# Kernel tuning notes

Measured on AMD Instinct MI355X. Metric: run time of the kernel, lower is better.

## Reference

```python
import jax, jax.numpy as jnp
import numpy as np

C, S, H = 64, 2048, 512
ITERATIONS = 3

def squash(x, eps=1e-07):
    # per-vector squash along last dim: (|x|^2/(1+|x|^2)) * x/|x|
    sq = jnp.sum(x * x, axis=-1, keepdims=True)
    safe_norm = jnp.sqrt(sq + eps)
    scale = sq / (1.0 + sq)
    return scale * (x / safe_norm)

def setup_inputs() -> dict:
    key = jax.random.key(0)
    k1, k2 = jax.random.split(key)
    x = jax.random.normal(k1, (C * S, H), dtype=jnp.float32)
    # xavier-normal init for Linear(H, H)
    std = np.sqrt(2.0 / (H + H)).astype(np.float32)
    W_weight = jax.random.normal(k2, (H, H), dtype=jnp.float32) * std
    W_bias = jnp.zeros((H,), dtype=jnp.float32)
    return {"x": x, "W_weight": W_weight, "W_bias": W_bias}

def reference(x, W_weight, W_bias):
    xr = x.reshape(C, S, H)
    # e_ij = squash(Linear(x))  -> [C, S, H]
    e_ij = squash(jnp.einsum('csh,oh->cso', xr, W_weight) + W_bias)
    b_ij = jnp.zeros((C, S), dtype=x.dtype)
    c_i = jnp.zeros((C, H), dtype=x.dtype)
    for _ in range(ITERATIONS):
        d_i = jax.nn.softmax(b_ij, axis=1)[..., None]          # [C, S, 1]
        c_i = squash(jnp.sum(d_i * e_ij, axis=1))              # [C, H]
        b_ij = b_ij + jnp.einsum('csh,ch->cs', e_ij, c_i)      # [C, S]
    return c_i
```

## Files before the change

kernel.cpp:

```cpp
#include <hip/hip_runtime.h>
#include <hip/hip_fp16.h>

#define HDIM 512

typedef __fp16 fp16x2 __attribute__((ext_vector_type(2)));
typedef _Float16 h8 __attribute__((ext_vector_type(8)));
typedef __attribute__((ext_vector_type(4))) float floatx4;

__global__ __launch_bounds__(256) void prep_w_kernel(
    const float* __restrict__ W, _Float16* __restrict__ wf) {
  int i = (blockIdx.x * 256 + threadIdx.x) * 4;
  float4 f = *(const float4*)(W + i);
  wf[i + 0] = (_Float16)f.x;
  wf[i + 1] = (_Float16)f.y;
  wf[i + 2] = (_Float16)f.z;
  wf[i + 3] = (_Float16)f.w;
}

#define BM 128
#define BN 128
#define BK 64

__global__ __launch_bounds__(256) void gemm_kernel(
    const float* __restrict__ x, const _Float16* __restrict__ wf,
    const float* __restrict__ bias, __half* __restrict__ y,
    float* __restrict__ sq) {
  __shared__ _Float16 xs[BM * BK];
  __shared__ _Float16 wsm[BN * BK];

  const int tid = threadIdx.x;
  const int lane = tid & 63;
  const int widx = tid >> 6;
  const int wave_m = widx >> 1, wave_n = widx & 1;
  const int lrow = lane & 15, quad = lane >> 4, l7 = lane & 7;

  const int bid = blockIdx.x;
  const int m_blk = ((bid >> 5) << 3) + (bid & 7);
  const int n_blk = (bid >> 3) & 3;
  const int row0 = m_blk * BM;
  const int col0 = n_blk * BN;

  floatx4 acc[4][4];
#pragma unroll
  for (int i = 0; i < 4; ++i)
#pragma unroll
    for (int j = 0; j < 4; ++j) acc[i][j] = (floatx4){0.f, 0.f, 0.f, 0.f};

  const int xm = tid >> 3;
  const int xkg = tid & 7;
  const int wn_sub = lane >> 3;
  const int wphys = lane & 7;

  for (int kt = 0; kt < 8; ++kt) {
    const int k0 = kt * BK;
    __syncthreads();
#pragma unroll
    for (int p = 0; p < 4; ++p) {
      int m = p * 32 + xm;
      const float* gp = x + (size_t)(row0 + m) * HDIM + k0 + xkg * 8;
      float4 f0 = *(const float4*)gp;
      float4 f1 = *(const float4*)(gp + 4);
      union { h8 v8; fp16x2 v2[4]; } u;
      u.v2[0] = __builtin_amdgcn_cvt_pkrtz(f0.x, f0.y);
      u.v2[1] = __builtin_amdgcn_cvt_pkrtz(f0.z, f0.w);
      u.v2[2] = __builtin_amdgcn_cvt_pkrtz(f1.x, f1.y);
      u.v2[3] = __builtin_amdgcn_cvt_pkrtz(f1.z, f1.w);
      int phys = xkg ^ (m & 7);
      *(h8*)&xs[m * 64 + phys * 8] = u.v8;
    }
#pragma unroll
    for (int q = 0; q < 4; ++q) {
      int i = widx * 4 + q;
      int n_loc = 8 * i + wn_sub;
      int kg_l = wphys ^ (n_loc & 7);
      size_t goff = (size_t)(col0 + n_loc) * HDIM + k0 + kg_l * 8;
      __builtin_amdgcn_global_load_lds(
          (const __attribute__((address_space(1))) void*)(wf + goff),
          (__attribute__((address_space(3))) void*)&wsm[i * 512], 16, 0, 0);
    }
    __syncthreads();
#pragma unroll
    for (int ks = 0; ks < 2; ++ks) {
      int physA = (ks * 4 + quad) ^ l7;
      h8 a[4], bh[4];
#pragma unroll
      for (int mt = 0; mt < 4; ++mt) {
        int r = wave_m * 64 + mt * 16 + lrow;
        a[mt] = *(const h8*)&xs[r * 64 + physA * 8];
      }
#pragma unroll
      for (int nt = 0; nt < 4; ++nt) {
        int c = wave_n * 64 + nt * 16 + lrow;
        bh[nt] = *(const h8*)&wsm[c * 64 + physA * 8];
      }
#pragma unroll
      for (int mt = 0; mt < 4; ++mt)
#pragma unroll
        for (int nt = 0; nt < 4; ++nt)
          acc[mt][nt] = __builtin_amdgcn_mfma_f32_16x16x32_f16(
              a[mt], bh[nt], acc[mt][nt], 0, 0, 0);
    }
  }

  int colg[4];
  float bias_v[4];
#pragma unroll
  for (int nt = 0; nt < 4; ++nt) {
    colg[nt] = col0 + wave_n * 64 + nt * 16 + lrow;
    bias_v[nt] = bias[colg[nt]];
  }
#pragma unroll
  for (int mt = 0; mt < 4; ++mt) {
#pragma unroll
    for (int r = 0; r < 4; ++r) {
      int rowg = row0 + wave_m * 64 + mt * 16 + quad * 4 + r;
      float s = 0.f;
#pragma unroll
      for (int nt = 0; nt < 4; ++nt) {
        float yv = acc[mt][nt][r] + bias_v[nt];
        s += yv * yv;
        y[(size_t)rowg * HDIM + colg[nt]] = __float2half(yv);
      }
      s += __shfl_xor(s, 1, 64);
      s += __shfl_xor(s, 2, 64);
      s += __shfl_xor(s, 4, 64);
      s += __shfl_xor(s, 8, 64);
      if (lrow == 0) atomicAdd(&sq[rowg], s);
    }
  }
}

__global__ __launch_bounds__(256) void kbv_kernel(
    const __half* __restrict__ y, const float* __restrict__ sqbuf,
    float* __restrict__ b, const float* __restrict__ c_buf,
    float* __restrict__ u_part, float* __restrict__ den_part) {
  const int wave_g = blockIdx.x * 4 + (threadIdx.x >> 6);
  const int lane = threadIdx.x & 63;
  const int cap = wave_g >> 6;
  const int chunk = wave_g & 63;
  const int r0 = cap * 2048 + chunk * 32;

  float c8[8];
  {
    const float4* cp = (const float4*)(c_buf + cap * HDIM + lane * 8);
    float4 ca = cp[0], cb = cp[1];
    c8[0] = ca.x; c8[1] = ca.y; c8[2] = ca.z; c8[3] = ca.w;
    c8[4] = cb.x; c8[5] = cb.y; c8[6] = cb.z; c8[7] = cb.w;
  }
  float u8[8] = {0, 0, 0, 0, 0, 0, 0, 0};
  float den = 0.f;

  union U { int4 v; __half hh[8]; };
  U cur[4], nxt[4];
  const __half* yb = y + (size_t)r0 * HDIM + lane * 8;
#pragma unroll
  for (int j = 0; j < 4; ++j) cur[j].v = *(const int4*)(yb + (size_t)j * HDIM);

  for (int g = 0; g < 8; ++g) {
    const int rg = r0 + g * 4;
    if (g < 7) {
#pragma unroll
      for (int j = 0; j < 4; ++j)
        nxt[j].v = *(const int4*)(yb + (size_t)(g * 4 + 4 + j) * HDIM);
    }
    float sc[4], bv[4];
#pragma unroll
    for (int j = 0; j < 4; ++j) {
      float s = sqbuf[rg + j];
      sc[j] = s / ((1.f + s) * sqrtf(s + 1e-7f));
      bv[j] = b[rg + j];
    }
    float dot[4];
#pragma unroll
    for (int j = 0; j < 4; ++j) {
      float d = 0.f;
#pragma unroll
      for (int k = 0; k < 8; ++k) d += __half2float(cur[j].hh[k]) * c8[k];
      dot[j] = d;
    }
#pragma unroll
    for (int s = 1; s < 64; s <<= 1) {
#pragma unroll
      for (int j = 0; j < 4; ++j) dot[j] += __shfl_xor(dot[j], s, 64);
    }
#pragma unroll
    for (int j = 0; j < 4; ++j) {
      float bn = bv[j] + sc[j] * dot[j];
      if (lane == 0) b[rg + j] = bn;
      float w = __expf(bn);
      den += w;
      float wsc = w * sc[j];
#pragma unroll
      for (int k = 0; k < 8; ++k) u8[k] += wsc * __half2float(cur[j].hh[k]);
    }
#pragma unroll
    for (int j = 0; j < 4; ++j) cur[j] = nxt[j];
  }
  float* up = u_part + (size_t)(cap * 64 + chunk) * HDIM + lane * 8;
  *(float4*)up = (float4){u8[0], u8[1], u8[2], u8[3]};
  *(float4*)(up + 4) = (float4){u8[4], u8[5], u8[6], u8[7]};
  if (lane == 0) den_part[cap * 64 + chunk] = den;
}

__global__ __launch_bounds__(512) void kcsq_kernel(
    const float* __restrict__ u_part, const float* __restrict__ den_part,
    float* __restrict__ out) {
  const int cap = blockIdx.x;
  const int t = threadIdx.x;
  __shared__ float red[512];

  float d = (t < 64) ? den_part[cap * 64 + t] : 0.f;
  red[t] = d;
  __syncthreads();
  for (int s = 256; s > 0; s >>= 1) {
    if (t < s) red[t] += red[t + s];
    __syncthreads();
  }
  const float den = red[0];
  __syncthreads();

  float v = 0.f;
  const float* up = u_part + (size_t)cap * 64 * HDIM + t;
  for (int ch = 0; ch < 64; ++ch) v += up[ch * HDIM];
  v /= den;

  red[t] = v * v;
  __syncthreads();
  for (int s = 256; s > 0; s >>= 1) {
    if (t < s) red[t] += red[t + s];
    __syncthreads();
  }
  const float sqv = red[0];
  const float scv = sqv / ((1.f + sqv) * sqrtf(sqv + 1e-7f));
  out[cap * HDIM + t] = v * scv;
}

extern "C" void kernel_launch(void* const* d_in, const int* in_sizes, int n_in,
                              void* d_out, int out_size, void* d_ws,
                              size_t ws_size, hipStream_t stream) {
  const float* x = (const float*)d_in[0];
  const float* W = (const float*)d_in[1];
  const float* bias = (const float*)d_in[2];
  float* out = (float*)d_out;
  char* ws = (char*)d_ws;

  __half* y = (__half*)ws;
  float* sq = (float*)(ws + (size_t)134217728);
  float* b = sq + 131072;
  float* c_buf = b + 131072;
  _Float16* wf = (_Float16*)(c_buf + 32768);
  float* u_part = (float*)(wf + 262144);
  float* den_part = u_part + (size_t)64 * 64 * 512;

  (void)hipMemsetAsync(sq, 0,
                       (size_t)(131072 + 131072 + 32768) * sizeof(float),
                       stream);

  prep_w_kernel<<<256, 256, 0, stream>>>(W, wf);
  gemm_kernel<<<4096, 256, 0, stream>>>(x, wf, bias, y, sq);

  for (int it = 0; it < 3; ++it) {
    kbv_kernel<<<1024, 256, 0, stream>>>(y, sq, b, c_buf, u_part, den_part);
    kcsq_kernel<<<64, 512, 0, stream>>>(u_part, den_part,
                                        (it == 2) ? out : c_buf);
  }
}
```

Before: 549.6 us.

## Prefetch next GEMM K-tile, widen kbv row batches, reduce partials in-block

The GEMM now double-buffers the weight tile in LDS and holds the next x tile in registers, so global loads for step k+1 overlap the MFMA work of step k. The routing kernel processes 8 rows per group, fully unrolled, which raises memory-level parallelism. It also sums its four waves' partial u vectors in shared memory before writing, which cuts the partial buffer and the final reduction by a factor of 4. The cost is more registers (prefetched x plus 8-row buffers) and more LDS, which may lower occupancy.

```diff
diff --git a/kernel.cpp b/kernel.cpp
--- a/kernel.cpp
+++ b/kernel.cpp
@@ -17,16 +17,12 @@
   wf[i + 3] = (_Float16)f.w;
 }
 
-#define BM 128
-#define BN 128
-#define BK 64
-
 __global__ __launch_bounds__(256) void gemm_kernel(
     const float* __restrict__ x, const _Float16* __restrict__ wf,
     const float* __restrict__ bias, __half* __restrict__ y,
     float* __restrict__ sq) {
-  __shared__ _Float16 xs[BM * BK];
-  __shared__ _Float16 wsm[BN * BK];
+  __shared__ _Float16 xs[128 * 64];
+  __shared__ _Float16 wsm[2][128 * 64];
 
   const int tid = threadIdx.x;
   const int lane = tid & 63;
@@ -37,8 +33,8 @@
   const int bid = blockIdx.x;
   const int m_blk = ((bid >> 5) << 3) + (bid & 7);
   const int n_blk = (bid >> 3) & 3;
-  const int row0 = m_blk * BM;
-  const int col0 = n_blk * BN;
+  const int row0 = m_blk * 128;
+  const int col0 = n_blk * 128;
 
   floatx4 acc[4][4];
 #pragma unroll
@@ -51,34 +47,60 @@
   const int wn_sub = lane >> 3;
   const int wphys = lane & 7;
 
+  float4 xr[4][2];
+  const float* xbase = x + (size_t)row0 * HDIM + xkg * 8;
+#pragma unroll
+  for (int p = 0; p < 4; ++p) {
+    const float* gp = xbase + (size_t)(p * 32 + xm) * HDIM;
+    xr[p][0] = *(const float4*)gp;
+    xr[p][1] = *(const float4*)(gp + 4);
+  }
+#pragma unroll
+  for (int q = 0; q < 4; ++q) {
+    int i = widx * 4 + q;
+    int n_loc = 8 * i + wn_sub;
+    int kg_l = wphys ^ (n_loc & 7);
+    size_t goff = (size_t)(col0 + n_loc) * HDIM + kg_l * 8;
+    __builtin_amdgcn_global_load_lds(
+        (const __attribute__((address_space(1))) void*)(wf + goff),
+        (__attribute__((address_space(3))) void*)&wsm[0][i * 512], 16, 0, 0);
+  }
+
   for (int kt = 0; kt < 8; ++kt) {
-    const int k0 = kt * BK;
     __syncthreads();
 #pragma unroll
     for (int p = 0; p < 4; ++p) {
       int m = p * 32 + xm;
-      const float* gp = x + (size_t)(row0 + m) * HDIM + k0 + xkg * 8;
-      float4 f0 = *(const float4*)gp;
-      float4 f1 = *(const float4*)(gp + 4);
       union { h8 v8; fp16x2 v2[4]; } u;
-      u.v2[0] = __builtin_amdgcn_cvt_pkrtz(f0.x, f0.y);
-      u.v2[1] = __builtin_amdgcn_cvt_pkrtz(f0.z, f0.w);
-      u.v2[2] = __builtin_amdgcn_cvt_pkrtz(f1.x, f1.y);
-      u.v2[3] = __builtin_amdgcn_cvt_pkrtz(f1.z, f1.w);
+      u.v2[0] = __builtin_amdgcn_cvt_pkrtz(xr[p][0].x, xr[p][0].y);
+      u.v2[1] = __builtin_amdgcn_cvt_pkrtz(xr[p][0].z, xr[p][0].w);
+      u.v2[2] = __builtin_amdgcn_cvt_pkrtz(xr[p][1].x, xr[p][1].y);
+      u.v2[3] = __builtin_amdgcn_cvt_pkrtz(xr[p][1].z, xr[p][1].w);
       int phys = xkg ^ (m & 7);
       *(h8*)&xs[m * 64 + phys * 8] = u.v8;
     }
-#pragma unroll
-    for (int q = 0; q < 4; ++q) {
-      int i = widx * 4 + q;
-      int n_loc = 8 * i + wn_sub;
-      int kg_l = wphys ^ (n_loc & 7);
-      size_t goff = (size_t)(col0 + n_loc) * HDIM + k0 + kg_l * 8;
-      __builtin_amdgcn_global_load_lds(
-          (const __attribute__((address_space(1))) void*)(wf + goff),
-          (__attribute__((address_space(3))) void*)&wsm[i * 512], 16, 0, 0);
-    }
     __syncthreads();
+    if (kt < 7) {
+      const int k1 = (kt + 1) * 64;
+      _Float16* wdst = &wsm[(kt + 1) & 1][0];
+#pragma unroll
+      for (int q = 0; q < 4; ++q) {
+        int i = widx * 4 + q;
+        int n_loc = 8 * i + wn_sub;
+        int kg_l = wphys ^ (n_loc & 7);
+        size_t goff = (size_t)(col0 + n_loc) * HDIM + k1 + kg_l * 8;
+        __builtin_amdgcn_global_load_lds(
+            (const __attribute__((address_space(1))) void*)(wf + goff),
+            (__attribute__((address_space(3))) void*)&wdst[i * 512], 16, 0, 0);
+      }
+#pragma unroll
+      for (int p = 0; p < 4; ++p) {
+        const float* gp = xbase + (size_t)(p * 32 + xm) * HDIM + k1;
+        xr[p][0] = *(const float4*)gp;
+        xr[p][1] = *(const float4*)(gp + 4);
+      }
+    }
+    const _Float16* wcur = &wsm[kt & 1][0];
 #pragma unroll
     for (int ks = 0; ks < 2; ++ks) {
       int physA = (ks * 4 + quad) ^ l7;
@@ -91,7 +113,7 @@
 #pragma unroll
       for (int nt = 0; nt < 4; ++nt) {
         int c = wave_n * 64 + nt * 16 + lrow;
-        bh[nt] = *(const h8*)&wsm[c * 64 + physA * 8];
+        bh[nt] = *(const h8*)&wcur[c * 64 + physA * 8];
       }
 #pragma unroll
       for (int mt = 0; mt < 4; ++mt)
@@ -134,8 +156,9 @@
     const __half* __restrict__ y, const float* __restrict__ sqbuf,
     float* __restrict__ b, const float* __restrict__ c_buf,
     float* __restrict__ u_part, float* __restrict__ den_part) {
-  const int wave_g = blockIdx.x * 4 + (threadIdx.x >> 6);
+  const int w = threadIdx.x >> 6;
   const int lane = threadIdx.x & 63;
+  const int wave_g = blockIdx.x * 4 + w;
   const int cap = wave_g >> 6;
   const int chunk = wave_g & 63;
   const int r0 = cap * 2048 + chunk * 32;
@@ -151,28 +174,29 @@
   float den = 0.f;
 
   union U { int4 v; __half hh[8]; };
-  U cur[4], nxt[4];
+  U cur[8], nxt[8];
   const __half* yb = y + (size_t)r0 * HDIM + lane * 8;
 #pragma unroll
-  for (int j = 0; j < 4; ++j) cur[j].v = *(const int4*)(yb + (size_t)j * HDIM);
-
-  for (int g = 0; g < 8; ++g) {
-    const int rg = r0 + g * 4;
-    if (g < 7) {
-#pragma unroll
-      for (int j = 0; j < 4; ++j)
-        nxt[j].v = *(const int4*)(yb + (size_t)(g * 4 + 4 + j) * HDIM);
-    }
-    float sc[4], bv[4];
-#pragma unroll
-    for (int j = 0; j < 4; ++j) {
+  for (int j = 0; j < 8; ++j) cur[j].v = *(const int4*)(yb + (size_t)j * HDIM);
+
+#pragma unroll
+  for (int g = 0; g < 4; ++g) {
+    const int rg = r0 + g * 8;
+    if (g < 3) {
+#pragma unroll
+      for (int j = 0; j < 8; ++j)
+        nxt[j].v = *(const int4*)(yb + (size_t)(g * 8 + 8 + j) * HDIM);
+    }
+    float sc[8], bv[8];
+#pragma unroll
+    for (int j = 0; j < 8; ++j) {
       float s = sqbuf[rg + j];
       sc[j] = s / ((1.f + s) * sqrtf(s + 1e-7f));
       bv[j] = b[rg + j];
     }
-    float dot[4];
-#pragma unroll
-    for (int j = 0; j < 4; ++j) {
+    float dot[8];
+#pragma unroll
+    for (int j = 0; j < 8; ++j) {
       float d = 0.f;
 #pragma unroll
       for (int k = 0; k < 8; ++k) d += __half2float(cur[j].hh[k]) * c8[k];
@@ -181,25 +205,38 @@
 #pragma unroll
     for (int s = 1; s < 64; s <<= 1) {
 #pragma unroll
-      for (int j = 0; j < 4; ++j) dot[j] += __shfl_xor(dot[j], s, 64);
-    }
-#pragma unroll
-    for (int j = 0; j < 4; ++j) {
+      for (int j = 0; j < 8; ++j) dot[j] += __shfl_xor(dot[j], s, 64);
+    }
+#pragma unroll
+    for (int j = 0; j < 8; ++j) {
       float bn = bv[j] + sc[j] * dot[j];
       if (lane == 0) b[rg + j] = bn;
-      float w = __expf(bn);
-      den += w;
-      float wsc = w * sc[j];
+      float wj = __expf(bn);
+      den += wj;
+      float wsc = wj * sc[j];
 #pragma unroll
       for (int k = 0; k < 8; ++k) u8[k] += wsc * __half2float(cur[j].hh[k]);
     }
 #pragma unroll
-    for (int j = 0; j < 4; ++j) cur[j] = nxt[j];
-  }
-  float* up = u_part + (size_t)(cap * 64 + chunk) * HDIM + lane * 8;
-  *(float4*)up = (float4){u8[0], u8[1], u8[2], u8[3]};
-  *(float4*)(up + 4) = (float4){u8[4], u8[5], u8[6], u8[7]};
-  if (lane == 0) den_part[cap * 64 + chunk] = den;
+    for (int j = 0; j < 8; ++j) cur[j] = nxt[j];
+  }
+
+  __shared__ float lred[4][512];
+  __shared__ float ldn[4];
+#pragma unroll
+  for (int k = 0; k < 8; ++k) lred[w][lane * 8 + k] = u8[k];
+  if (lane == 0) ldn[w] = den;
+  __syncthreads();
+  const int t = threadIdx.x;
+  const int blkc = blockIdx.x & 15;
+#pragma unroll
+  for (int hh = 0; hh < 2; ++hh) {
+    int h = hh * 256 + t;
+    float v = lred[0][h] + lred[1][h] + lred[2][h] + lred[3][h];
+    u_part[((size_t)cap * 16 + blkc) * HDIM + h] = v;
+  }
+  if (t == 0)
+    den_part[cap * 16 + blkc] = ldn[0] + ldn[1] + ldn[2] + ldn[3];
 }
 
 __global__ __launch_bounds__(512) void kcsq_kernel(
@@ -208,20 +245,23 @@
   const int cap = blockIdx.x;
   const int t = threadIdx.x;
   __shared__ float red[512];
-
-  float d = (t < 64) ? den_part[cap * 64 + t] : 0.f;
-  red[t] = d;
+  __shared__ float sden;
+
+  if (t < 16) red[t] = den_part[cap * 16 + t];
   __syncthreads();
-  for (int s = 256; s > 0; s >>= 1) {
-    if (t < s) red[t] += red[t + s];
-    __syncthreads();
-  }
-  const float den = red[0];
+  if (t == 0) {
+    float s = 0.f;
+#pragma unroll
+    for (int i = 0; i < 16; ++i) s += red[i];
+    sden = s;
+  }
   __syncthreads();
+  const float den = sden;
 
   float v = 0.f;
-  const float* up = u_part + (size_t)cap * 64 * HDIM + t;
-  for (int ch = 0; ch < 64; ++ch) v += up[ch * HDIM];
+  const float* up = u_part + (size_t)cap * 16 * HDIM + t;
+#pragma unroll
+  for (int ch = 0; ch < 16; ++ch) v += up[ch * HDIM];
   v /= den;
 
   red[t] = v * v;
@@ -250,7 +290,7 @@
   float* c_buf = b + 131072;
   _Float16* wf = (_Float16*)(c_buf + 32768);
   float* u_part = (float*)(wf + 262144);
-  float* den_part = u_part + (size_t)64 * 64 * 512;
+  float* den_part = u_part + (size_t)64 * 16 * 512;
 
   (void)hipMemsetAsync(sq, 0,
                        (size_t)(131072 + 131072 + 32768) * sizeof(float),
```

Measured after the change: 565.8 us. 2.9% more time.
